# Kernel optimization log

Measured on AMD Instinct MI355X. Metric: run time of the kernel, lower is better.

The kernel has to match this reference:

```python
import jax, jax.numpy as jnp
import numpy as np

OUT = 7          # out_size
SCALE = 0.125    # spatial_scale (1/8, FPN P3)
SAMPLES = 2      # sample_num


def setup_inputs() -> dict:
    key = jax.random.key(0)
    k1, k2, k3, k4, k5, k6, k7, k8, k9 = jax.random.split(key, 9)
    B, C, H, W = 2, 256, 256, 256
    n = 1024
    features = jax.random.normal(k1, (B, C, H, W), jnp.float32)
    # rois: (batch_idx, cx, cy, w, h, theta) in IMAGE coordinates
    bidx = jax.random.randint(k2, (n,), 0, B).astype(jnp.float32)
    cx = jax.random.uniform(k3, (n,), jnp.float32, 0.0, W / SCALE)
    cy = jax.random.uniform(k4, (n,), jnp.float32, 0.0, H / SCALE)
    rw = jax.random.uniform(k5, (n,), jnp.float32, 16.0, 512.0)
    rh = jax.random.uniform(k6, (n,), jnp.float32, 16.0, 512.0)
    ang = jax.random.uniform(k7, (n,), jnp.float32, -np.pi, np.pi)
    rois = jnp.stack([bidx, cx, cy, rw, rh, ang], axis=1)
    ic = OUT * OUT * C  # 12544
    fc = 1024
    w1 = jax.random.normal(k8, (ic, fc), jnp.float32) * 0.01
    b1 = jnp.zeros((fc,), jnp.float32)
    w2 = jax.random.normal(k9, (fc, OUT * OUT), jnp.float32) * 0.01
    b2 = jnp.zeros((OUT * OUT,), jnp.float32)
    return {"features": features, "rois": rois, "w1": w1, "b1": b1, "w2": w2, "b2": b2}


def _roi_align_rotated(features, rois):
    B, C, H, W = features.shape
    n = rois.shape[0]
    bidx = rois[:, 0].astype(jnp.int32)
    cx = rois[:, 1] * SCALE
    cy = rois[:, 2] * SCALE
    rw = jnp.maximum(rois[:, 3] * SCALE, 1.0)
    rh = jnp.maximum(rois[:, 4] * SCALE, 1.0)
    theta = rois[:, 5]
    bin_w = rw / OUT
    bin_h = rh / OUT
    g = jnp.arange(OUT, dtype=features.dtype)
    s = (jnp.arange(SAMPLES, dtype=features.dtype) + 0.5) / SAMPLES
    # roi-local sample coordinates: [n, OUT, SAMPLES]
    yy = -rh[:, None, None] / 2 + (g[None, :, None] + s[None, None, :]) * bin_h[:, None, None]
    xx = -rw[:, None, None] / 2 + (g[None, :, None] + s[None, None, :]) * bin_w[:, None, None]
    # broadcast to [n, oh, ow, sy, sx]
    yy = yy[:, :, None, :, None]
    xx = xx[:, None, :, None, :]
    ct = jnp.cos(theta)[:, None, None, None, None]
    st = jnp.sin(theta)[:, None, None, None, None]
    xs = xx * ct - yy * st + cx[:, None, None, None, None]
    ys = xx * st + yy * ct + cy[:, None, None, None, None]
    shp = (n, OUT, OUT, SAMPLES, SAMPLES)
    xs = jnp.broadcast_to(xs, shp).reshape(n, -1)  # [n, P], P = OUT*OUT*S*S
    ys = jnp.broadcast_to(ys, shp).reshape(n, -1)
    valid = (ys > -1.0) & (ys < H) & (xs > -1.0) & (xs < W)
    ysc = jnp.clip(ys, 0.0, H - 1)
    xsc = jnp.clip(xs, 0.0, W - 1)
    yl = jnp.floor(ysc).astype(jnp.int32)
    xl = jnp.floor(xsc).astype(jnp.int32)
    yh = jnp.minimum(yl + 1, H - 1)
    xh = jnp.minimum(xl + 1, W - 1)
    ly = ysc - yl
    lx = xsc - xl
    hy = 1.0 - ly
    hx = 1.0 - lx
    be = jnp.broadcast_to(bidx[:, None], yl.shape)
    # bilinear gathers: each [n, P, C]
    v11 = features[be, :, yl, xl]
    v12 = features[be, :, yl, xh]
    v21 = features[be, :, yh, xl]
    v22 = features[be, :, yh, xh]
    val = ((hy * hx)[..., None] * v11 + (hy * lx)[..., None] * v12
           + (ly * hx)[..., None] * v21 + (ly * lx)[..., None] * v22)
    val = val * valid[..., None].astype(val.dtype)
    # average the SAMPLES*SAMPLES points per bin -> [n, OUT, OUT, C]
    val = val.reshape(n, OUT, OUT, SAMPLES * SAMPLES, C).mean(axis=3)
    return jnp.transpose(val, (0, 3, 1, 2))  # [n, C, OUT, OUT]


def reference(features, rois, w1, b1, w2, b2):
    n = rois.shape[0]
    x = _roi_align_rotated(features, rois)          # [n, C, OUT, OUT]
    flat = x.reshape(n, -1)                          # [n, C*OUT*OUT]
    hid = jax.nn.relu(flat @ w1 + b1)
    mask = jax.nn.sigmoid(hid @ w2 + b2).reshape(n, 1, OUT, OUT)
    return x * mask
```

## Files before the change

kernel.cpp:

```cpp
#include <hip/hip_runtime.h>
#include <hip/hip_bf16.h>

typedef unsigned short u16;
typedef unsigned int u32;
typedef short short8 __attribute__((ext_vector_type(8)));
typedef float f32x4 __attribute__((ext_vector_type(4)));

#define OUTD 7
#define NROI 1024
#define CH 256
#define KDIM 12544
#define NHID 1024
#define KSPLIT 8

__device__ __forceinline__ float bf_lo(u32 u) {
    union { u32 i; float f; } v; v.i = u << 16; return v.f;
}
__device__ __forceinline__ float bf_hi(u32 u) {
    union { u32 i; float f; } v; v.i = u & 0xffff0000u; return v.f;
}
__device__ __forceinline__ u16 f2b(float f) {
    return (u16)(__bfloat16_as_ushort(__float2bfloat16(f)));
}
__device__ __forceinline__ void async16(const void* g, void* l) {
    __builtin_amdgcn_global_load_lds((const __attribute__((address_space(1))) u32*)g,
                                     (__attribute__((address_space(3))) u32*)l, 16, 0, 0);
}

__global__ __launch_bounds__(256) void transpose_feat(const float* __restrict__ f,
                                                      u16* __restrict__ ft) {
    __shared__ u32 tile[64 * 133];
    int pb = blockIdx.x;
    int b  = blockIdx.y;
    int tid = threadIdx.x;
    const float* src = f + (size_t)b * CH * 65536 + (size_t)pb * 64;
#pragma unroll
    for (int it = 0; it < 8; ++it) {
        int id = tid + 256 * it;
        int f4 = id & 15, c2 = id >> 4;
        const float* s0 = src + (size_t)(2 * c2) * 65536 + f4 * 4;
        float4 a = *(const float4*)(s0);
        float4 bb = *(const float4*)(s0 + 65536);
#pragma unroll
        for (int j = 0; j < 4; ++j) {
            float av = (&a.x)[j], bv = (&bb.x)[j];
            tile[(f4 * 4 + j) * 133 + c2] = (u32)f2b(av) | ((u32)f2b(bv) << 16);
        }
    }
    __syncthreads();
    u16* dst = ft + ((size_t)b * 65536 + (size_t)pb * 64) * CH;
#pragma unroll
    for (int it = 0; it < 16; ++it) {
        int px = it * 4 + (tid >> 6);
        int cg = tid & 63;
        uint2 o;
        o.x = tile[px * 133 + cg * 2];
        o.y = tile[px * 133 + cg * 2 + 1];
        *(uint2*)(dst + (size_t)px * CH + cg * 4) = o;
    }
}

__global__ __launch_bounds__(256) void transpose_w1(const float* __restrict__ w1,
                                                    u16* __restrict__ w1t) {
    __shared__ float tile[32][129];
    int kb = blockIdx.x;
    int nb = blockIdx.y;
    int tid = threadIdx.x;
#pragma unroll
    for (int i = 0; i < 4; ++i) {
        int id = tid + 256 * i;
        int r = id >> 3, f4 = id & 7;
        float4 v = *(const float4*)(w1 + (size_t)(kb * 128 + r) * NHID + nb * 32 + f4 * 4);
        tile[f4 * 4 + 0][r] = v.x;
        tile[f4 * 4 + 1][r] = v.y;
        tile[f4 * 4 + 2][r] = v.z;
        tile[f4 * 4 + 3][r] = v.w;
    }
    __syncthreads();
#pragma unroll
    for (int i = 0; i < 4; ++i) {
        int id = tid + 256 * i;
        int nn = id >> 5, kg = id & 31;
        uint2 o;
        o.x = (u32)f2b(tile[nn][kg * 4 + 0]) | ((u32)f2b(tile[nn][kg * 4 + 1]) << 16);
        o.y = (u32)f2b(tile[nn][kg * 4 + 2]) | ((u32)f2b(tile[nn][kg * 4 + 3]) << 16);
        *(uint2*)(w1t + (size_t)(nb * 32 + nn) * KDIM + kb * 128 + kg * 4) = o;
    }
}

__global__ __launch_bounds__(256) void transpose_w2(const float* __restrict__ w2,
                                                    float* __restrict__ w2t) {
    int j = blockIdx.x;
    for (int k = threadIdx.x; k < NHID; k += 256)
        w2t[(size_t)j * NHID + k] = w2[(size_t)k * 49 + j];
}

__global__ __launch_bounds__(256) void roi_align(const u16* __restrict__ ft,
                                                 const float* __restrict__ rois,
                                                 u16* __restrict__ flat) {
    __shared__ u16 sbuf[49 * 260];
    int i = blockIdx.x;
    int tid = threadIdx.x;
    int lane = tid & 63, w = tid >> 6;
    float r0 = rois[i * 6 + 0], r1 = rois[i * 6 + 1], r2 = rois[i * 6 + 2];
    float r3 = rois[i * 6 + 3], r4 = rois[i * 6 + 4], th = rois[i * 6 + 5];
    int b = (int)r0;
    float cx = r1 * 0.125f, cy = r2 * 0.125f;
    float rw = fmaxf(r3 * 0.125f, 1.0f), rh = fmaxf(r4 * 0.125f, 1.0f);
    float bw = rw * (1.0f / 7.0f), bh = rh * (1.0f / 7.0f);
    float ct = cosf(th), st = sinf(th);
    const u16* fb = ft + (size_t)b * 65536 * CH;
    int coff = lane * 4;

    int start = w * 12 + (w > 0 ? 1 : 0);
    int cnt = (w == 0) ? 13 : 12;
    for (int bi = 0; bi < cnt; ++bi) {
        int bin = start + bi;
        int ph = bin / 7, pw = bin - ph * 7;
        float a0 = 0.f, a1 = 0.f, a2 = 0.f, a3 = 0.f;
#pragma unroll
        for (int s = 0; s < 4; ++s) {
            int sy = s >> 1, sx2 = s & 1;
            float yy = -rh * 0.5f + ((float)ph + ((float)sy + 0.5f) * 0.5f) * bh;
            float xx = -rw * 0.5f + ((float)pw + ((float)sx2 + 0.5f) * 0.5f) * bw;
            float xs = xx * ct - yy * st + cx;
            float ys = xx * st + yy * ct + cy;
            bool valid = (ys > -1.0f) && (ys < 256.0f) && (xs > -1.0f) && (xs < 256.0f);
            float ysc = fminf(fmaxf(ys, 0.f), 255.f);
            float xsc = fminf(fmaxf(xs, 0.f), 255.f);
            int yl = (int)floorf(ysc), xl = (int)floorf(xsc);
            int yh = min(yl + 1, 255), xh = min(xl + 1, 255);
            float ly = ysc - (float)yl, lx = xsc - (float)xl;
            float hy = 1.f - ly, hx = 1.f - lx;
            float w11 = hy * hx, w12 = hy * lx, w21 = ly * hx, w22 = ly * lx;
            if (!valid) { w11 = w12 = w21 = w22 = 0.f; }
            uint2 v11 = *(const uint2*)(fb + (((size_t)yl * 256 + xl) << 8) + coff);
            uint2 v12 = *(const uint2*)(fb + (((size_t)yl * 256 + xh) << 8) + coff);
            uint2 v21 = *(const uint2*)(fb + (((size_t)yh * 256 + xl) << 8) + coff);
            uint2 v22 = *(const uint2*)(fb + (((size_t)yh * 256 + xh) << 8) + coff);
            a0 += w11 * bf_lo(v11.x) + w12 * bf_lo(v12.x) + w21 * bf_lo(v21.x) + w22 * bf_lo(v22.x);
            a1 += w11 * bf_hi(v11.x) + w12 * bf_hi(v12.x) + w21 * bf_hi(v21.x) + w22 * bf_hi(v22.x);
            a2 += w11 * bf_lo(v11.y) + w12 * bf_lo(v12.y) + w21 * bf_lo(v21.y) + w22 * bf_lo(v22.y);
            a3 += w11 * bf_hi(v11.y) + w12 * bf_hi(v12.y) + w21 * bf_hi(v21.y) + w22 * bf_hi(v22.y);
        }
        uint2 o;
        o.x = (u32)f2b(a0 * 0.25f) | ((u32)f2b(a1 * 0.25f) << 16);
        o.y = (u32)f2b(a2 * 0.25f) | ((u32)f2b(a3 * 0.25f) << 16);
        *(uint2*)(sbuf + bin * 260 + coff) = o;
    }
    __syncthreads();
    uint2* fl = (uint2*)(flat + (size_t)i * KDIM);
#pragma unroll 1
    for (int k = tid; k < 3136; k += 256) {
        int e = k * 4;
        int c = e / 49, bn = e - c * 49;
        u16 r0_ = sbuf[bn * 260 + c]; if (++bn == 49) { bn = 0; ++c; }
        u16 r1_ = sbuf[bn * 260 + c]; if (++bn == 49) { bn = 0; ++c; }
        u16 r2_ = sbuf[bn * 260 + c]; if (++bn == 49) { bn = 0; ++c; }
        u16 r3_ = sbuf[bn * 260 + c];
        uint2 o;
        o.x = (u32)r0_ | ((u32)r1_ << 16);
        o.y = (u32)r2_ | ((u32)r3_ << 16);
        fl[k] = o;
    }
}

__global__ __launch_bounds__(256) void gemm1(const u16* __restrict__ A,
                                             const u16* __restrict__ Bt,
                                             float* __restrict__ part) {
    const int K = KDIM;
    int nb = blockIdx.x, mb = blockIdx.y, ks = blockIdx.z;
    int steps = 24 + (ks < 4 ? 1 : 0);
    int kbase = (ks * 24 + (ks < 4 ? ks : 4)) * 64;
    __shared__ __align__(16) u16 As[2][128 * 64];
    __shared__ __align__(16) u16 Bs[2][128 * 64];
    int tid = threadIdx.x;
    int lane = tid & 63, w = tid >> 6;
    int wm = w >> 1, wn = w & 1;
    f32x4 acc[4][4] = {};
    const u16* Ab = A + (size_t)(mb * 128) * K;
    const u16* Bb = Bt + (size_t)(nb * 128) * K;

    auto stage = [&](int buf, int kk) {
#pragma unroll
        for (int j = 0; j < 4; ++j) {
            int c = w * 4 + j;
            int cid = c * 64 + lane;
            int row = cid >> 3, pq = cid & 7;
            int q = pq ^ (row & 7);
            async16(Ab + (size_t)row * K + kk + q * 8, &As[buf][c * 512 + lane * 8]);
            async16(Bb + (size_t)row * K + kk + q * 8, &Bs[buf][c * 512 + lane * 8]);
        }
    };

    stage(0, kbase);
    int cur = 0;
    for (int s = 0; s < steps; ++s) {
        if (s + 1 < steps) {
            stage(cur ^ 1, kbase + (s + 1) * 64);
            asm volatile("s_waitcnt vmcnt(8)" ::: "memory");
        } else {
            asm volatile("s_waitcnt vmcnt(0)" ::: "memory");
        }
        __builtin_amdgcn_s_barrier();
        const u16* Asb = &As[cur][0];
        const u16* Bsb = &Bs[cur][0];
#pragma unroll
        for (int kh = 0; kh < 2; ++kh) {
            short8 af[4], bf[4];
#pragma unroll
            for (int t = 0; t < 4; ++t) {
                int q = kh * 4 + (lane >> 4);
                int r = wm * 64 + t * 16 + (lane & 15);
                int pq = q ^ (r & 7);
                af[t] = *(const short8*)(Asb + r * 64 + pq * 8);
                int rb = wn * 64 + t * 16 + (lane & 15);
                int pqb = q ^ (rb & 7);
                bf[t] = *(const short8*)(Bsb + rb * 64 + pqb * 8);
            }
#pragma unroll
            for (int mt = 0; mt < 4; ++mt)
#pragma unroll
                for (int nt = 0; nt < 4; ++nt)
                    acc[mt][nt] = __builtin_amdgcn_mfma_f32_16x16x32_bf16(af[mt], bf[nt], acc[mt][nt], 0, 0, 0);
        }
        __builtin_amdgcn_s_barrier();
        cur ^= 1;
    }
    float* P = part + (size_t)ks * NROI * NHID;
    int m_base = mb * 128 + wm * 64, n_base = nb * 128 + wn * 64;
#pragma unroll
    for (int mt = 0; mt < 4; ++mt)
#pragma unroll
        for (int nt = 0; nt < 4; ++nt)
#pragma unroll
            for (int i = 0; i < 4; ++i) {
                int m = m_base + mt * 16 + (lane >> 4) * 4 + i;
                int n = n_base + nt * 16 + (lane & 15);
                P[(size_t)m * NHID + n] = acc[mt][nt][i];
            }
}

__global__ __launch_bounds__(256) void gemm2_apply(const float* __restrict__ part,
                                                   const float* __restrict__ b1,
                                                   const float* __restrict__ w2t,
                                                   const float* __restrict__ b2,
                                                   const u16* __restrict__ flat,
                                                   float* __restrict__ out) {
    __shared__ __align__(16) float hrow[NHID];
    __shared__ float partial[256];
    __shared__ float mrow[49];
    int i = blockIdx.x;
    int tid = threadIdx.x;
    {
        float4 s = ((const float4*)b1)[tid];
        size_t base = (size_t)i * 256 + tid;
#pragma unroll
        for (int j = 0; j < KSPLIT; ++j) {
            float4 p = ((const float4*)part)[(size_t)j * 262144 + base];
            s.x += p.x; s.y += p.y; s.z += p.z; s.w += p.w;
        }
        float4 r;
        r.x = fmaxf(s.x, 0.f); r.y = fmaxf(s.y, 0.f);
        r.z = fmaxf(s.z, 0.f); r.w = fmaxf(s.w, 0.f);
        ((float4*)hrow)[tid] = r;
    }
    __syncthreads();
    float p = 0.f;
    if (tid < 245) {
        int j = tid / 5, kc = tid - (tid / 5) * 5;
        int k0 = (256 * kc) / 5, k1 = (256 * (kc + 1)) / 5;
        const float4* wv = (const float4*)(w2t + (size_t)j * NHID);
        const float4* hv = (const float4*)hrow;
        for (int k = k0; k < k1; ++k) {
            float4 a = hv[k], b = wv[k];
            p += a.x * b.x + a.y * b.y + a.z * b.z + a.w * b.w;
        }
    }
    partial[tid] = p;
    __syncthreads();
    if (tid < 49) {
        float s = b2[tid];
#pragma unroll
        for (int q = 0; q < 5; ++q) s += partial[tid * 5 + q];
        mrow[tid] = 1.f / (1.f + expf(-s));
    }
    __syncthreads();
    const uint2* fl = (const uint2*)(flat + (size_t)i * KDIM);
    float4* op = (float4*)(out + (size_t)i * KDIM);
#pragma unroll 1
    for (int idx = tid; idx < 3136; idx += 256) {
        uint2 v = fl[idx];
        int e = idx * 4;
        int pp = e - (e / 49) * 49;
        float4 r;
        r.x = bf_lo(v.x) * mrow[pp]; if (++pp == 49) pp = 0;
        r.y = bf_hi(v.x) * mrow[pp]; if (++pp == 49) pp = 0;
        r.z = bf_lo(v.y) * mrow[pp]; if (++pp == 49) pp = 0;
        r.w = bf_hi(v.y) * mrow[pp];
        op[idx] = r;
    }
}

extern "C" void kernel_launch(void* const* d_in, const int* in_sizes, int n_in,
                              void* d_out, int out_size, void* d_ws, size_t ws_size,
                              hipStream_t stream) {
    const float* features = (const float*)d_in[0];
    const float* rois     = (const float*)d_in[1];
    const float* w1       = (const float*)d_in[2];
    const float* b1       = (const float*)d_in[3];
    const float* w2       = (const float*)d_in[4];
    const float* b2       = (const float*)d_in[5];
    float* out = (float*)d_out;
    char* ws = (char*)d_ws;

    u16* featT  = (u16*)(ws);
    u16* flat   = (u16*)(ws + 67108864);
    u16* w1t    = (u16*)(ws + 92798976);
    float* part = (float*)(ws + 118489088);
    float* w2t  = (float*)(ws + 152043520);

    transpose_feat<<<dim3(1024, 2), 256, 0, stream>>>(features, featT);
    transpose_w1<<<dim3(98, 32), 256, 0, stream>>>(w1, w1t);
    transpose_w2<<<49, 256, 0, stream>>>(w2, w2t);
    roi_align<<<NROI, 256, 0, stream>>>(featT, rois, flat);
    gemm1<<<dim3(8, 8, KSPLIT), 256, 0, stream>>>(flat, w1t, part);
    gemm2_apply<<<NROI, 256, 0, stream>>>(part, b1, w2t, b2, flat, out);
}
```

Measured before the change: 387.4 us.

## Fuse prep transposes into one launch and retile gemm1 to 256x256 blocks

The three preprocessing kernels (feature transpose, w1 transpose/convert, w2 transpose) become one kernel that dispatches on block index, removing two launches and the serialization between them. gemm1 moves from 128x128 tiles with 256 threads and split-K 8 to 256x256 tiles with 512 threads and split-K 14, with an even 14-step K range per split. Each wave now computes 128x64 of output, which raises operand reuse per LDS load. The trade-offs are higher LDS and register use, only 224 blocks to fill the device, and more split-K partials for gemm2_apply to read and sum.

```diff
diff --git a/kernel.cpp b/kernel.cpp
--- a/kernel.cpp
+++ b/kernel.cpp
@@ -11,7 +11,7 @@
 #define CH 256
 #define KDIM 12544
 #define NHID 1024
-#define KSPLIT 8
+#define KSPLIT 14
 
 __device__ __forceinline__ float bf_lo(u32 u) {
     union { u32 i; float f; } v; v.i = u << 16; return v.f;
@@ -27,72 +27,72 @@
                                      (__attribute__((address_space(3))) u32*)l, 16, 0, 0);
 }
 
-__global__ __launch_bounds__(256) void transpose_feat(const float* __restrict__ f,
-                                                      u16* __restrict__ ft) {
-    __shared__ u32 tile[64 * 133];
-    int pb = blockIdx.x;
-    int b  = blockIdx.y;
+__global__ __launch_bounds__(256) void prep(const float* __restrict__ f,
+                                            const float* __restrict__ w1,
+                                            const float* __restrict__ w2,
+                                            u16* __restrict__ ft,
+                                            u16* __restrict__ w1t,
+                                            float* __restrict__ w2t) {
+    __shared__ u32 smem[64 * 133];
+    int bid = blockIdx.x;
     int tid = threadIdx.x;
-    const float* src = f + (size_t)b * CH * 65536 + (size_t)pb * 64;
-#pragma unroll
-    for (int it = 0; it < 8; ++it) {
-        int id = tid + 256 * it;
-        int f4 = id & 15, c2 = id >> 4;
-        const float* s0 = src + (size_t)(2 * c2) * 65536 + f4 * 4;
-        float4 a = *(const float4*)(s0);
-        float4 bb = *(const float4*)(s0 + 65536);
-#pragma unroll
-        for (int j = 0; j < 4; ++j) {
-            float av = (&a.x)[j], bv = (&bb.x)[j];
-            tile[(f4 * 4 + j) * 133 + c2] = (u32)f2b(av) | ((u32)f2b(bv) << 16);
-        }
-    }
-    __syncthreads();
-    u16* dst = ft + ((size_t)b * 65536 + (size_t)pb * 64) * CH;
-#pragma unroll
-    for (int it = 0; it < 16; ++it) {
-        int px = it * 4 + (tid >> 6);
-        int cg = tid & 63;
-        uint2 o;
-        o.x = tile[px * 133 + cg * 2];
-        o.y = tile[px * 133 + cg * 2 + 1];
-        *(uint2*)(dst + (size_t)px * CH + cg * 4) = o;
-    }
-}
-
-__global__ __launch_bounds__(256) void transpose_w1(const float* __restrict__ w1,
-                                                    u16* __restrict__ w1t) {
-    __shared__ float tile[32][129];
-    int kb = blockIdx.x;
-    int nb = blockIdx.y;
-    int tid = threadIdx.x;
-#pragma unroll
-    for (int i = 0; i < 4; ++i) {
-        int id = tid + 256 * i;
-        int r = id >> 3, f4 = id & 7;
-        float4 v = *(const float4*)(w1 + (size_t)(kb * 128 + r) * NHID + nb * 32 + f4 * 4);
-        tile[f4 * 4 + 0][r] = v.x;
-        tile[f4 * 4 + 1][r] = v.y;
-        tile[f4 * 4 + 2][r] = v.z;
-        tile[f4 * 4 + 3][r] = v.w;
-    }
-    __syncthreads();
-#pragma unroll
-    for (int i = 0; i < 4; ++i) {
-        int id = tid + 256 * i;
-        int nn = id >> 5, kg = id & 31;
-        uint2 o;
-        o.x = (u32)f2b(tile[nn][kg * 4 + 0]) | ((u32)f2b(tile[nn][kg * 4 + 1]) << 16);
-        o.y = (u32)f2b(tile[nn][kg * 4 + 2]) | ((u32)f2b(tile[nn][kg * 4 + 3]) << 16);
-        *(uint2*)(w1t + (size_t)(nb * 32 + nn) * KDIM + kb * 128 + kg * 4) = o;
-    }
-}
-
-__global__ __launch_bounds__(256) void transpose_w2(const float* __restrict__ w2,
-                                                    float* __restrict__ w2t) {
-    int j = blockIdx.x;
-    for (int k = threadIdx.x; k < NHID; k += 256)
-        w2t[(size_t)j * NHID + k] = w2[(size_t)k * 49 + j];
+    if (bid < 2048) {
+        int pb = bid >> 1;
+        int b  = bid & 1;
+        const float* src = f + (size_t)b * CH * 65536 + (size_t)pb * 64;
+#pragma unroll
+        for (int it = 0; it < 8; ++it) {
+            int id = tid + 256 * it;
+            int f4 = id & 15, c2 = id >> 4;
+            const float* s0 = src + (size_t)(2 * c2) * 65536 + f4 * 4;
+            float4 a = *(const float4*)(s0);
+            float4 bb = *(const float4*)(s0 + 65536);
+#pragma unroll
+            for (int j = 0; j < 4; ++j) {
+                float av = (&a.x)[j], bv = (&bb.x)[j];
+                smem[(f4 * 4 + j) * 133 + c2] = (u32)f2b(av) | ((u32)f2b(bv) << 16);
+            }
+        }
+        __syncthreads();
+        u16* dst = ft + ((size_t)b * 65536 + (size_t)pb * 64) * CH;
+#pragma unroll
+        for (int it = 0; it < 16; ++it) {
+            int px = it * 4 + (tid >> 6);
+            int cg = tid & 63;
+            uint2 o;
+            o.x = smem[px * 133 + cg * 2];
+            o.y = smem[px * 133 + cg * 2 + 1];
+            *(uint2*)(dst + (size_t)px * CH + cg * 4) = o;
+        }
+    } else if (bid < 5184) {
+        int t = bid - 2048;
+        int kb = t % 98, nb = t / 98;
+        float (*tile)[129] = (float(*)[129])smem;
+#pragma unroll
+        for (int i = 0; i < 4; ++i) {
+            int id = tid + 256 * i;
+            int r = id >> 3, f4 = id & 7;
+            float4 v = *(const float4*)(w1 + (size_t)(kb * 128 + r) * NHID + nb * 32 + f4 * 4);
+            tile[f4 * 4 + 0][r] = v.x;
+            tile[f4 * 4 + 1][r] = v.y;
+            tile[f4 * 4 + 2][r] = v.z;
+            tile[f4 * 4 + 3][r] = v.w;
+        }
+        __syncthreads();
+#pragma unroll
+        for (int i = 0; i < 4; ++i) {
+            int id = tid + 256 * i;
+            int nn = id >> 5, kg = id & 31;
+            uint2 o;
+            o.x = (u32)f2b(tile[nn][kg * 4 + 0]) | ((u32)f2b(tile[nn][kg * 4 + 1]) << 16);
+            o.y = (u32)f2b(tile[nn][kg * 4 + 2]) | ((u32)f2b(tile[nn][kg * 4 + 3]) << 16);
+            *(uint2*)(w1t + (size_t)(nb * 32 + nn) * KDIM + kb * 128 + kg * 4) = o;
+        }
+    } else {
+        int j = bid - 5184;
+        for (int k = tid; k < NHID; k += 256)
+            w2t[(size_t)j * NHID + k] = w2[(size_t)k * 49 + j];
+    }
 }
 
 __global__ __launch_bounds__(256) void roi_align(const u16* __restrict__ ft,
@@ -165,21 +165,21 @@
     }
 }
 
-__global__ __launch_bounds__(256) void gemm1(const u16* __restrict__ A,
+__global__ __launch_bounds__(512) void gemm1(const u16* __restrict__ A,
                                              const u16* __restrict__ Bt,
                                              float* __restrict__ part) {
     const int K = KDIM;
     int nb = blockIdx.x, mb = blockIdx.y, ks = blockIdx.z;
-    int steps = 24 + (ks < 4 ? 1 : 0);
-    int kbase = (ks * 24 + (ks < 4 ? ks : 4)) * 64;
-    __shared__ __align__(16) u16 As[2][128 * 64];
-    __shared__ __align__(16) u16 Bs[2][128 * 64];
+    const int steps = 14;
+    int kbase = ks * 896;
+    __shared__ __align__(16) u16 As[2][256 * 64];
+    __shared__ __align__(16) u16 Bs[2][256 * 64];
     int tid = threadIdx.x;
     int lane = tid & 63, w = tid >> 6;
-    int wm = w >> 1, wn = w & 1;
-    f32x4 acc[4][4] = {};
-    const u16* Ab = A + (size_t)(mb * 128) * K;
-    const u16* Bb = Bt + (size_t)(nb * 128) * K;
+    int wm = w >> 2, wn = w & 3;
+    f32x4 acc[8][4] = {};
+    const u16* Ab = A + (size_t)(mb * 256) * K;
+    const u16* Bb = Bt + (size_t)(nb * 256) * K;
 
     auto stage = [&](int buf, int kk) {
 #pragma unroll
@@ -207,19 +207,22 @@
         const u16* Bsb = &Bs[cur][0];
 #pragma unroll
         for (int kh = 0; kh < 2; ++kh) {
-            short8 af[4], bf[4];
-#pragma unroll
-            for (int t = 0; t < 4; ++t) {
-                int q = kh * 4 + (lane >> 4);
-                int r = wm * 64 + t * 16 + (lane & 15);
+            short8 af[8], bf[4];
+            int q = kh * 4 + (lane >> 4);
+#pragma unroll
+            for (int t = 0; t < 8; ++t) {
+                int r = wm * 128 + t * 16 + (lane & 15);
                 int pq = q ^ (r & 7);
                 af[t] = *(const short8*)(Asb + r * 64 + pq * 8);
+            }
+#pragma unroll
+            for (int t = 0; t < 4; ++t) {
                 int rb = wn * 64 + t * 16 + (lane & 15);
                 int pqb = q ^ (rb & 7);
                 bf[t] = *(const short8*)(Bsb + rb * 64 + pqb * 8);
             }
 #pragma unroll
-            for (int mt = 0; mt < 4; ++mt)
+            for (int mt = 0; mt < 8; ++mt)
 #pragma unroll
                 for (int nt = 0; nt < 4; ++nt)
                     acc[mt][nt] = __builtin_amdgcn_mfma_f32_16x16x32_bf16(af[mt], bf[nt], acc[mt][nt], 0, 0, 0);
@@ -228,9 +231,9 @@
         cur ^= 1;
     }
     float* P = part + (size_t)ks * NROI * NHID;
-    int m_base = mb * 128 + wm * 64, n_base = nb * 128 + wn * 64;
-#pragma unroll
-    for (int mt = 0; mt < 4; ++mt)
+    int m_base = mb * 256 + wm * 128, n_base = nb * 256 + wn * 64;
+#pragma unroll
+    for (int mt = 0; mt < 8; ++mt)
 #pragma unroll
         for (int nt = 0; nt < 4; ++nt)
 #pragma unroll
@@ -318,12 +321,10 @@
     u16* flat   = (u16*)(ws + 67108864);
     u16* w1t    = (u16*)(ws + 92798976);
     float* part = (float*)(ws + 118489088);
-    float* w2t  = (float*)(ws + 152043520);
-
-    transpose_feat<<<dim3(1024, 2), 256, 0, stream>>>(features, featT);
-    transpose_w1<<<dim3(98, 32), 256, 0, stream>>>(w1, w1t);
-    transpose_w2<<<49, 256, 0, stream>>>(w2, w2t);
+    float* w2t  = (float*)(ws + 177209344);
+
+    prep<<<5233, 256, 0, stream>>>(features, w1, w2, featT, w1t, w2t);
     roi_align<<<NROI, 256, 0, stream>>>(featT, rois, flat);
-    gemm1<<<dim3(8, 8, KSPLIT), 256, 0, stream>>>(flat, w1t, part);
+    gemm1<<<dim3(4, 4, KSPLIT), 512, 0, stream>>>(flat, w1t, part);
     gemm2_apply<<<NROI, 256, 0, stream>>>(part, b1, w2t, b2, flat, out);
 }
```

Measured after the change: 388.4 us. Within noise of the previous version (+0.2%).
